# Kernel optimization log

Measured on AMD Instinct MI355X. Metric: run time of the kernel, lower is better.

Reference implementation:

```python
import jax, jax.numpy as jnp
import numpy as np

NUM_EMBEDDINGS = 1024
EMBEDDING_DIM = 64
COMMITMENT_COST = 0.25
EPS_NORM = 1e-12  # torch F.normalize eps


def _l2_normalize(x):
    n = jnp.linalg.norm(x, axis=-1, keepdims=True)
    return x / jnp.maximum(n, EPS_NORM)


def setup_inputs() -> dict:
    key = jax.random.key(0)
    k1, k2 = jax.random.split(key)
    inputs = jax.random.normal(k1, (16, 4096, EMBEDDING_DIM), dtype=jnp.float32)
    weight = jax.random.normal(k2, (NUM_EMBEDDINGS, EMBEDDING_DIM), dtype=jnp.float32) * 0.02
    return {"inputs": inputs, "weight": weight}


def reference(inputs, weight):
    input_shape = inputs.shape
    x = _l2_normalize(inputs)                      # [B,S,D]
    flat = x.reshape(-1, EMBEDDING_DIM)            # [N,D]
    w = _l2_normalize(weight)                      # [K,D]

    distances = (jnp.sum(flat ** 2, axis=1, keepdims=True)
                 + jnp.sum(w ** 2, axis=1)
                 - 2.0 * flat @ w.T)               # [N,K]
    encoding_indices = jnp.argmin(distances, axis=1)  # [N]

    quantized = w[encoding_indices].reshape(input_shape)  # [B,S,D]

    e_latent_loss = jnp.mean((jax.lax.stop_gradient(quantized) - x) ** 2)
    q_latent_loss = jnp.mean((quantized - jax.lax.stop_gradient(x)) ** 2)
    loss = q_latent_loss + COMMITMENT_COST * e_latent_loss

    # straight-through estimator
    quantized_ste = x + jax.lax.stop_gradient(quantized - x)

    # perplexity (no-grad bookkeeping)
    n = encoding_indices.shape[0]
    counts = jnp.zeros((NUM_EMBEDDINGS,), jnp.float32).at[encoding_indices].add(1.0)
    avg_probs = counts / n
    perplexity = jnp.exp(-jnp.sum(avg_probs * jnp.log(avg_probs + 1e-10)))

    return loss, quantized_ste, perplexity, encoding_indices[:, None]
```

## Files before the change

kernel.cpp:

```cpp
#include <hip/hip_runtime.h>
#include <hip/hip_bf16.h>
#include <math.h>

#define NROWS   65536
#define DIM     64
#define KCODES  1024
#define RPB     128
#define NBLOCKS (NROWS / RPB)

#define NEXACT 9u

typedef short short8 __attribute__((ext_vector_type(8)));
typedef float f32x4  __attribute__((ext_vector_type(4)));

#define OUT_Q_OFF    ((size_t)1)
#define OUT_PERP_OFF ((size_t)(1 + (size_t)NROWS * DIM))
#define OUT_IDX_OFF  ((size_t)(2 + (size_t)NROWS * DIM))

#define WS_COUNTS 0
#define WS_SSEC   4096
#define WS_DONE   4100
#define WS_WN     8192
#define WS_SK     (WS_WN + KCODES*DIM*4)
#define WS_WNH    (WS_SK + KCODES*4)
#define WS_WNL    (WS_WNH + KCODES*DIM*2)

__device__ __forceinline__ unsigned short bf16_rne(float f) {
  unsigned u = __float_as_uint(f);
  return (unsigned short)((u + 0x7FFFu + ((u >> 16) & 1u)) >> 16);
}
__device__ __forceinline__ float bf16f(unsigned short h) {
  return __uint_as_float(((unsigned)h) << 16);
}
__device__ __forceinline__ unsigned med3u(unsigned a, unsigned b, unsigned c) {
  unsigned d;
  asm("v_med3_u32 %0, %1, %2, %3" : "=v"(d) : "v"(a), "v"(b), "v"(c));
  return d;
}

__global__ void __launch_bounds__(64) normalize_w_kernel(
    const float* __restrict__ w, float* __restrict__ wn, float* __restrict__ sk,
    unsigned short* __restrict__ wnh, unsigned short* __restrict__ wnl,
    unsigned* __restrict__ counts, float* __restrict__ sse_accum,
    unsigned* __restrict__ done) {
  const int k = blockIdx.x;
  const int d = threadIdx.x;
  if (d == 0) {
    counts[k] = 0u;
    if (k == 0) { *sse_accum = 0.f; *done = 0u; }
  }
  float v = w[k * DIM + d];
  float ss = v * v;
  #pragma unroll
  for (int o = 32; o > 0; o >>= 1) ss += __shfl_xor(ss, o, 64);
  const float den = fmaxf(sqrtf(ss), 1e-12f);
  const float q = v / den;
  wn[k * DIM + d] = q;
  const unsigned short h = bf16_rne(q);
  wnh[k * DIM + d] = h;
  wnl[k * DIM + d] = bf16_rne(q - bf16f(h));
  float s2 = q * q;
  #pragma unroll
  for (int o = 32; o > 0; o >>= 1) s2 += __shfl_xor(s2, o, 64);
  if (d == 0) sk[k] = s2;
}

__global__ void __launch_bounds__(256) vq_mega_kernel(
    const float* __restrict__ x, const unsigned short* __restrict__ wnh,
    const unsigned short* __restrict__ wnl, const float* __restrict__ sk,
    const float* __restrict__ wn, float* __restrict__ out,
    unsigned* __restrict__ counts, float* __restrict__ sse_accum,
    unsigned* __restrict__ done) {
  __shared__ unsigned AB[9216];
  __shared__ float skb[2][64];
  __shared__ float c_arr[RPB];
  __shared__ float rowsse[RPB];
  __shared__ int   ib[RPB];
  __shared__ int   qlist[RPB];
  __shared__ int   flist[RPB];
  __shared__ int   qn_s, fn_s;
  __shared__ int   islast;
  const int tid = threadIdx.x;
  const int lane = tid & 63, wave = tid >> 6;

  if (tid == 0) { qn_s = 0; fn_s = 0; }

  {
    const int row_l = tid >> 1;
    const int half = tid & 1;
    const size_t row = (size_t)blockIdx.x * RPB + row_l;
    const float4* xr = (const float4*)(x + row * DIM) + half * 8;
    float4 xv[8];
    float ss = 0.f;
    #pragma unroll
    for (int i = 0; i < 8; i++) {
      xv[i] = xr[i];
      ss += xv[i].x * xv[i].x + xv[i].y * xv[i].y + xv[i].z * xv[i].z + xv[i].w * xv[i].w;
    }
    ss += __shfl_xor(ss, 1, 64);
    const float inv = 1.0f / fmaxf(sqrtf(ss), 1e-12f);
    float c = 0.f;
    #pragma unroll
    for (int i = 0; i < 8; i++) {
      const float a0 = xv[i].x * inv, a1 = xv[i].y * inv;
      const float a2 = xv[i].z * inv, a3 = xv[i].w * inv;
      c += a0 * a0 + a1 * a1 + a2 * a2 + a3 * a3;
      const unsigned short h0 = bf16_rne(a0), h1 = bf16_rne(a1);
      const unsigned short h2 = bf16_rne(a2), h3 = bf16_rne(a3);
      const unsigned short l0 = bf16_rne(a0 - bf16f(h0)), l1 = bf16_rne(a1 - bf16f(h1));
      const unsigned short l2 = bf16_rne(a2 - bf16f(h2)), l3 = bf16_rne(a3 - bf16f(h3));
      AB[row_l * 36 + half * 16 + 2 * i]            = (unsigned)h0 | ((unsigned)h1 << 16);
      AB[row_l * 36 + half * 16 + 2 * i + 1]        = (unsigned)h2 | ((unsigned)h3 << 16);
      AB[4608 + row_l * 36 + half * 16 + 2 * i]     = (unsigned)l0 | ((unsigned)l1 << 16);
      AB[4608 + row_l * 36 + half * 16 + 2 * i + 1] = (unsigned)l2 | ((unsigned)l3 << 16);
    }
    c += __shfl_xor(c, 1, 64);
    if (half == 0) c_arr[row_l] = c;
  }
  __syncthreads();

  short8 ah[2][2], al[2][2];
  #pragma unroll
  for (int rt = 0; rt < 2; rt++)
    #pragma unroll
    for (int kk = 0; kk < 2; kk++) {
      const int r = wave * 32 + rt * 16 + (lane & 15);
      ah[rt][kk] = *(const short8*)&AB[r * 36 + kk * 16 + (lane >> 4) * 4];
      al[rt][kk] = *(const short8*)&AB[4608 + r * 36 + kk * 16 + (lane >> 4) * 4];
    }
  __syncthreads();

  unsigned k1[8], k2[8], k3[8];
  #pragma unroll
  for (int s = 0; s < 8; s++) { k1[s] = 0xFFFFFFFFu; k2[s] = 0xFFFFFFFFu; k3[s] = 0xFFFFFFFFu; }

  {
    const int code = tid >> 2, q = tid & 3;
    const float4* gh = (const float4*)(wnh + (size_t)code * DIM + q * 16);
    const float4* gl = (const float4*)(wnl + (size_t)code * DIM + q * 16);
    float4* dh = (float4*)&AB[code * 36 + q * 8];
    float4* dl = (float4*)&AB[2304 + code * 36 + q * 8];
    dh[0] = gh[0]; dh[1] = gh[1];
    dl[0] = gl[0]; dl[1] = gl[1];
    if (tid < 64) skb[0][tid] = sk[tid] + 4.0f;
  }

  #pragma unroll 2
  for (int c = 0; c < 16; c++) {
    const int b = c & 1;
    __syncthreads();
    if (c < 15) {
      const int nb = b ^ 1;
      const int code = tid >> 2, q = tid & 3;
      const float4* gh = (const float4*)(wnh + (size_t)((c + 1) * 64 + code) * DIM + q * 16);
      const float4* gl = (const float4*)(wnl + (size_t)((c + 1) * 64 + code) * DIM + q * 16);
      float4* dh = (float4*)&AB[nb * 4608 + code * 36 + q * 8];
      float4* dl = (float4*)&AB[nb * 4608 + 2304 + code * 36 + q * 8];
      dh[0] = gh[0]; dh[1] = gh[1];
      dl[0] = gl[0]; dl[1] = gl[1];
      if (tid < 64) skb[nb][tid] = sk[(c + 1) * 64 + tid] + 4.0f;
    }
    #pragma unroll
    for (int tt = 0; tt < 4; tt++) {
      const int cb = tt * 16 + (lane & 15);
      const float skv4 = skb[b][cb];
      const unsigned chi = (unsigned)(c * 4 + tt);
      const short8 bh0 = *(const short8*)&AB[b * 4608 + cb * 36 + 0 * 16 + (lane >> 4) * 4];
      const short8 bh1 = *(const short8*)&AB[b * 4608 + cb * 36 + 1 * 16 + (lane >> 4) * 4];
      const short8 bl0 = *(const short8*)&AB[b * 4608 + 2304 + cb * 36 + 0 * 16 + (lane >> 4) * 4];
      const short8 bl1 = *(const short8*)&AB[b * 4608 + 2304 + cb * 36 + 1 * 16 + (lane >> 4) * 4];
      #pragma unroll
      for (int rt = 0; rt < 2; rt++) {
        f32x4 acc = {0.f, 0.f, 0.f, 0.f};
        acc = __builtin_amdgcn_mfma_f32_16x16x32_bf16(ah[rt][0], bh0, acc, 0, 0, 0);
        acc = __builtin_amdgcn_mfma_f32_16x16x32_bf16(ah[rt][1], bh1, acc, 0, 0, 0);
        acc = __builtin_amdgcn_mfma_f32_16x16x32_bf16(al[rt][0], bh0, acc, 0, 0, 0);
        acc = __builtin_amdgcn_mfma_f32_16x16x32_bf16(al[rt][1], bh1, acc, 0, 0, 0);
        acc = __builtin_amdgcn_mfma_f32_16x16x32_bf16(ah[rt][0], bl0, acc, 0, 0, 0);
        acc = __builtin_amdgcn_mfma_f32_16x16x32_bf16(ah[rt][1], bl1, acc, 0, 0, 0);
        #pragma unroll
        for (int i = 0; i < 4; i++) {
          const float dist4 = fmaf(-2.0f, acc[i], skv4);
          const unsigned key = (__float_as_uint(dist4) & 0xFFFFFFC0u) | chi;
          const int s = rt * 4 + i;
          const unsigned t = (k1[s] > key) ? k1[s] : key;
          k3[s] = med3u(k2[s], k3[s], t);
          k2[s] = med3u(k1[s], k2[s], key);
          k1[s] = (key < k1[s]) ? key : k1[s];
        }
      }
    }
  }

  #pragma unroll
  for (int s = 0; s < 8; s++) {
    unsigned a1 = (k1[s] << 4) | (unsigned)(lane & 15);
    unsigned a2 = (k2[s] << 4) | (unsigned)(lane & 15);
    unsigned a3 = (k3[s] << 4) | (unsigned)(lane & 15);
    #pragma unroll
    for (int m = 1; m < 16; m <<= 1) {
      const unsigned p1 = (unsigned)__shfl_xor((int)a1, m, 64);
      const unsigned p2 = (unsigned)__shfl_xor((int)a2, m, 64);
      const unsigned p3 = (unsigned)__shfl_xor((int)a3, m, 64);
      const unsigned th = (a1 > p1) ? a1 : p1;
      const unsigned n1 = (a1 < p1) ? a1 : p1;
      const unsigned m2 = (a2 < p2) ? a2 : p2;
      const unsigned m3 = (a3 < p3) ? a3 : p3;
      const unsigned hi = (th > m2) ? th : m2;
      a1 = n1;
      a2 = (th < m2) ? th : m2;
      const unsigned md = med3u(th, m2, m3);
      a3 = (hi < md) ? hi : md;
    }
    if ((lane & 15) == 0) {
      const int row_local = wave * 32 + (s >> 2) * 16 + (lane >> 4) * 4 + (s & 3);
      const int i1 = (int)(a1 & 1023u);
      ib[row_local] = i1;
      const unsigned ub = ((a1 & 0xFFFFFC00u) >> 4) | 0x40000000u;
      rowsse[row_local] = __uint_as_float(ub) - 4.0f + c_arr[row_local] + 1.6e-5f;
      const unsigned b1 = a1 >> 10, b2 = a2 >> 10, b3 = a3 >> 10;
      if (b3 - b1 < NEXACT) {
        flist[atomicAdd(&fn_s, 1)] = row_local;
      } else if (b2 - b1 < NEXACT) {
        qlist[atomicAdd(&qn_s, 1)] = row_local | (i1 << 7) | ((int)(a2 & 1023u) << 17);
      }
    }
  }
  __syncthreads();

  const int qn = qn_s, fn = fn_s;
  if (tid < qn) {
    const int packed = qlist[tid];
    const int rl = packed & 127;
    const int c1 = (packed >> 7) & 1023, c2i = (packed >> 17) & 1023;
    const size_t row = (size_t)blockIdx.x * RPB + rl;
    const float4* xr = (const float4*)(x + row * DIM);
    float4 xv[16];
    float ss = 0.f;
    #pragma unroll
    for (int i = 0; i < 16; i++) {
      xv[i] = xr[i];
      ss += xv[i].x * xv[i].x + xv[i].y * xv[i].y + xv[i].z * xv[i].z + xv[i].w * xv[i].w;
    }
    const float den = fmaxf(sqrtf(ss), 1e-12f);
    #pragma unroll
    for (int i = 0; i < 16; i++) { xv[i].x /= den; xv[i].y /= den; xv[i].z /= den; xv[i].w /= den; }
    float cc = 0.f;
    #pragma unroll
    for (int i = 0; i < 16; i++)
      cc += xv[i].x * xv[i].x + xv[i].y * xv[i].y + xv[i].z * xv[i].z + xv[i].w * xv[i].w;
    float dd[2]; const int cand[2] = {c1, c2i};
    #pragma unroll
    for (int t = 0; t < 2; t++) {
      const float4* wr = (const float4*)(wn + (size_t)cand[t] * DIM);
      float e0 = 0.f, e1 = 0.f, e2 = 0.f, e3 = 0.f;
      #pragma unroll
      for (int i = 0; i < 16; i++) {
        const float4 wv = wr[i];
        e0 = fmaf(xv[i].x, wv.x, e0);
        e1 = fmaf(xv[i].y, wv.y, e1);
        e2 = fmaf(xv[i].z, wv.z, e2);
        e3 = fmaf(xv[i].w, wv.w, e3);
      }
      dd[t] = (cc + sk[cand[t]]) - 2.0f * ((e0 + e1) + (e2 + e3));
    }
    const bool tb = (dd[1] < dd[0]) || (dd[1] == dd[0] && c2i < c1);
    ib[rl] = tb ? c2i : c1;
    rowsse[rl] = tb ? dd[1] : dd[0];
  }

  for (int qi = wave; qi < fn; qi += 4) {
    const int rl = flist[qi];
    const size_t row = (size_t)blockIdx.x * RPB + rl;
    const float4* xr = (const float4*)(x + row * DIM);
    float4 xv[16];
    float ss = 0.f;
    #pragma unroll
    for (int i = 0; i < 16; i++) {
      xv[i] = xr[i];
      ss += xv[i].x * xv[i].x + xv[i].y * xv[i].y + xv[i].z * xv[i].z + xv[i].w * xv[i].w;
    }
    const float den = fmaxf(sqrtf(ss), 1e-12f);
    #pragma unroll
    for (int i = 0; i < 16; i++) { xv[i].x /= den; xv[i].y /= den; xv[i].z /= den; xv[i].w /= den; }
    float cc = 0.f;
    #pragma unroll
    for (int i = 0; i < 16; i++)
      cc += xv[i].x * xv[i].x + xv[i].y * xv[i].y + xv[i].z * xv[i].z + xv[i].w * xv[i].w;

    float best = INFINITY;
    int bidx = 0x7FFFFFFF;
    for (int j = 0; j < 16; j++) {
      const int k = j * 64 + lane;
      const float4* wr = (const float4*)(wn + (size_t)k * DIM);
      float e0 = 0.f, e1 = 0.f, e2 = 0.f, e3 = 0.f;
      #pragma unroll
      for (int i = 0; i < 16; i++) {
        const float4 wv = wr[i];
        e0 = fmaf(xv[i].x, wv.x, e0);
        e1 = fmaf(xv[i].y, wv.y, e1);
        e2 = fmaf(xv[i].z, wv.z, e2);
        e3 = fmaf(xv[i].w, wv.w, e3);
      }
      const float dot = (e0 + e1) + (e2 + e3);
      const float dist = (cc + sk[k]) - 2.0f * dot;
      if (dist < best) { best = dist; bidx = k; }
    }
    #pragma unroll
    for (int m = 1; m < 64; m <<= 1) {
      const float pb = __shfl_xor(best, m, 64);
      const int pi = __shfl_xor(bidx, m, 64);
      if (pb < best || (pb == best && pi < bidx)) { best = pb; bidx = pi; }
    }
    if (lane == 0) { ib[rl] = bidx; rowsse[rl] = best; }
  }
  __syncthreads();

  if (tid < RPB) {
    const size_t row = (size_t)blockIdx.x * RPB + tid;
    const int idx = ib[tid];
    out[OUT_IDX_OFF + row] = (float)idx;
    atomicAdd(&counts[idx], 1u);
  }

  const size_t obase = OUT_Q_OFF + (size_t)blockIdx.x * (RPB * DIM);
  #pragma unroll 4
  for (int j = 0; j < 32; j++) {
    const int e = j * 256 + tid;
    out[obase + e] = wn[(size_t)ib[e >> 6] * DIM + (e & 63)];
  }

  __syncthreads();
  for (int s = 64; s > 0; s >>= 1) {
    if (tid < s) rowsse[tid] += rowsse[tid + s];
    __syncthreads();
  }
  if (tid == 0) atomicAdd(sse_accum, rowsse[0]);

  if (tid == 0) {
    __threadfence();
    islast = (atomicAdd(done, 1u) == NBLOCKS - 1) ? 1 : 0;
  }
  __syncthreads();
  if (islast) {
    __threadfence();
    float h = 0.f;
    #pragma unroll
    for (int i = 0; i < 4; i++) {
      const float cv = (float)counts[tid * 4 + i];
      const float avg = cv * (1.0f / (float)NROWS);
      h += avg * logf(avg + 1e-10f);
    }
    #pragma unroll
    for (int o = 32; o > 0; o >>= 1) h += __shfl_xor(h, o, 64);
    __shared__ float hred[4];
    if (lane == 0) hred[wave] = h;
    __syncthreads();
    if (tid == 0) {
      const float H = -(hred[0] + hred[1] + hred[2] + hred[3]);
      const float mse = *sse_accum * (1.0f / (float)((size_t)NROWS * DIM));
      out[0] = mse + 0.25f * mse;
      out[OUT_PERP_OFF] = expf(H);
    }
  }
}

extern "C" void kernel_launch(void* const* d_in, const int* in_sizes, int n_in,
                              void* d_out, int out_size, void* d_ws, size_t ws_size,
                              hipStream_t stream) {
  const float* x = (const float*)d_in[0];
  const float* w = (const float*)d_in[1];
  float* out = (float*)d_out;

  char* ws = (char*)d_ws;
  unsigned* counts    = (unsigned*)(ws + WS_COUNTS);
  float* sse_accum    = (float*)(ws + WS_SSEC);
  unsigned* done      = (unsigned*)(ws + WS_DONE);
  float* wn           = (float*)(ws + WS_WN);
  float* sk           = (float*)(ws + WS_SK);
  unsigned short* wnh = (unsigned short*)(ws + WS_WNH);
  unsigned short* wnl = (unsigned short*)(ws + WS_WNL);

  normalize_w_kernel<<<KCODES, 64, 0, stream>>>(w, wn, sk, wnh, wnl,
                                                counts, sse_accum, done);
  vq_mega_kernel<<<NBLOCKS, 256, 0, stream>>>(
      x, wnh, wnl, sk, wn, out, counts, sse_accum, done);
}
```

Before: 130.0 us.

## Double block to 512 threads, split codebook columns across wave pairs

Raises the block size from 256 to 512 threads. Each pair of waves now shares a row group, and each wave in the pair scans half of every 64-code chunk. The per-wave top-3 candidate keys are merged through shared memory in a new combine step before rows are classified for exact refinement. Loading and writeback loops are re-split across the extra threads. The goal is more waves per block to hide MFMA and LDS latency and to halve each wave's serial work, at the cost of an extra barrier, a merge pass, and possibly lower register budget under launch bounds of 4.

```diff
diff --git a/kernel.cpp b/kernel.cpp
--- a/kernel.cpp
+++ b/kernel.cpp
@@ -6,6 +6,7 @@
 #define DIM     64
 #define KCODES  1024
 #define RPB     128
+#define TPB     512
 #define NBLOCKS (NROWS / RPB)
 
 #define NEXACT 9u
@@ -37,6 +38,8 @@
   asm("v_med3_u32 %0, %1, %2, %3" : "=v"(d) : "v"(a), "v"(b), "v"(c));
   return d;
 }
+__device__ __forceinline__ unsigned uminu(unsigned a, unsigned b) { return a < b ? a : b; }
+__device__ __forceinline__ unsigned umaxu(unsigned a, unsigned b) { return a > b ? a : b; }
 
 __global__ void __launch_bounds__(64) normalize_w_kernel(
     const float* __restrict__ w, float* __restrict__ wn, float* __restrict__ sk,
@@ -65,13 +68,13 @@
   if (d == 0) sk[k] = s2;
 }
 
-__global__ void __launch_bounds__(256) vq_mega_kernel(
+__global__ void __launch_bounds__(TPB, 4) vq_mega_kernel(
     const float* __restrict__ x, const unsigned short* __restrict__ wnh,
     const unsigned short* __restrict__ wnl, const float* __restrict__ sk,
     const float* __restrict__ wn, float* __restrict__ out,
     unsigned* __restrict__ counts, float* __restrict__ sse_accum,
     unsigned* __restrict__ done) {
-  __shared__ unsigned AB[9216];
+  __shared__ __align__(16) unsigned AB[9216];
   __shared__ float skb[2][64];
   __shared__ float c_arr[RPB];
   __shared__ float rowsse[RPB];
@@ -80,28 +83,30 @@
   __shared__ int   flist[RPB];
   __shared__ int   qn_s, fn_s;
   __shared__ int   islast;
+  __shared__ float hred[8];
   const int tid = threadIdx.x;
   const int lane = tid & 63, wave = tid >> 6;
+  const int rg = wave >> 1, cg = wave & 1;
 
   if (tid == 0) { qn_s = 0; fn_s = 0; }
 
   {
-    const int row_l = tid >> 1;
-    const int half = tid & 1;
+    const int row_l = tid >> 2;
+    const int qr = tid & 3;
     const size_t row = (size_t)blockIdx.x * RPB + row_l;
-    const float4* xr = (const float4*)(x + row * DIM) + half * 8;
-    float4 xv[8];
+    const float4* xr = (const float4*)(x + row * DIM) + qr * 4;
+    float4 xv[4];
     float ss = 0.f;
     #pragma unroll
-    for (int i = 0; i < 8; i++) {
+    for (int i = 0; i < 4; i++) {
       xv[i] = xr[i];
       ss += xv[i].x * xv[i].x + xv[i].y * xv[i].y + xv[i].z * xv[i].z + xv[i].w * xv[i].w;
     }
-    ss += __shfl_xor(ss, 1, 64);
+    ss += __shfl_xor(ss, 1, 64); ss += __shfl_xor(ss, 2, 64);
     const float inv = 1.0f / fmaxf(sqrtf(ss), 1e-12f);
     float c = 0.f;
     #pragma unroll
-    for (int i = 0; i < 8; i++) {
+    for (int i = 0; i < 4; i++) {
       const float a0 = xv[i].x * inv, a1 = xv[i].y * inv;
       const float a2 = xv[i].z * inv, a3 = xv[i].w * inv;
       c += a0 * a0 + a1 * a1 + a2 * a2 + a3 * a3;
@@ -109,13 +114,13 @@
       const unsigned short h2 = bf16_rne(a2), h3 = bf16_rne(a3);
       const unsigned short l0 = bf16_rne(a0 - bf16f(h0)), l1 = bf16_rne(a1 - bf16f(h1));
       const unsigned short l2 = bf16_rne(a2 - bf16f(h2)), l3 = bf16_rne(a3 - bf16f(h3));
-      AB[row_l * 36 + half * 16 + 2 * i]            = (unsigned)h0 | ((unsigned)h1 << 16);
-      AB[row_l * 36 + half * 16 + 2 * i + 1]        = (unsigned)h2 | ((unsigned)h3 << 16);
-      AB[4608 + row_l * 36 + half * 16 + 2 * i]     = (unsigned)l0 | ((unsigned)l1 << 16);
-      AB[4608 + row_l * 36 + half * 16 + 2 * i + 1] = (unsigned)l2 | ((unsigned)l3 << 16);
-    }
-    c += __shfl_xor(c, 1, 64);
-    if (half == 0) c_arr[row_l] = c;
+      AB[row_l * 36 + qr * 8 + 2 * i]            = (unsigned)h0 | ((unsigned)h1 << 16);
+      AB[row_l * 36 + qr * 8 + 2 * i + 1]        = (unsigned)h2 | ((unsigned)h3 << 16);
+      AB[4608 + row_l * 36 + qr * 8 + 2 * i]     = (unsigned)l0 | ((unsigned)l1 << 16);
+      AB[4608 + row_l * 36 + qr * 8 + 2 * i + 1] = (unsigned)l2 | ((unsigned)l3 << 16);
+    }
+    c += __shfl_xor(c, 1, 64); c += __shfl_xor(c, 2, 64);
+    if (qr == 0) c_arr[row_l] = c;
   }
   __syncthreads();
 
@@ -124,7 +129,7 @@
   for (int rt = 0; rt < 2; rt++)
     #pragma unroll
     for (int kk = 0; kk < 2; kk++) {
-      const int r = wave * 32 + rt * 16 + (lane & 15);
+      const int r = rg * 32 + rt * 16 + (lane & 15);
       ah[rt][kk] = *(const short8*)&AB[r * 36 + kk * 16 + (lane >> 4) * 4];
       al[rt][kk] = *(const short8*)&AB[4608 + r * 36 + kk * 16 + (lane >> 4) * 4];
     }
@@ -135,13 +140,9 @@
   for (int s = 0; s < 8; s++) { k1[s] = 0xFFFFFFFFu; k2[s] = 0xFFFFFFFFu; k3[s] = 0xFFFFFFFFu; }
 
   {
-    const int code = tid >> 2, q = tid & 3;
-    const float4* gh = (const float4*)(wnh + (size_t)code * DIM + q * 16);
-    const float4* gl = (const float4*)(wnl + (size_t)code * DIM + q * 16);
-    float4* dh = (float4*)&AB[code * 36 + q * 8];
-    float4* dl = (float4*)&AB[2304 + code * 36 + q * 8];
-    dh[0] = gh[0]; dh[1] = gh[1];
-    dl[0] = gl[0]; dl[1] = gl[1];
+    const int code = tid >> 3, q = tid & 7;
+    *(float4*)&AB[code * 36 + q * 4]        = *(const float4*)(wnh + (size_t)code * DIM + q * 8);
+    *(float4*)&AB[2304 + code * 36 + q * 4] = *(const float4*)(wnl + (size_t)code * DIM + q * 8);
     if (tid < 64) skb[0][tid] = sk[tid] + 4.0f;
   }
 
@@ -151,20 +152,18 @@
     __syncthreads();
     if (c < 15) {
       const int nb = b ^ 1;
-      const int code = tid >> 2, q = tid & 3;
-      const float4* gh = (const float4*)(wnh + (size_t)((c + 1) * 64 + code) * DIM + q * 16);
-      const float4* gl = (const float4*)(wnl + (size_t)((c + 1) * 64 + code) * DIM + q * 16);
-      float4* dh = (float4*)&AB[nb * 4608 + code * 36 + q * 8];
-      float4* dl = (float4*)&AB[nb * 4608 + 2304 + code * 36 + q * 8];
-      dh[0] = gh[0]; dh[1] = gh[1];
-      dl[0] = gl[0]; dl[1] = gl[1];
+      const int code = tid >> 3, q = tid & 7;
+      *(float4*)&AB[nb * 4608 + code * 36 + q * 4] =
+          *(const float4*)(wnh + (size_t)((c + 1) * 64 + code) * DIM + q * 8);
+      *(float4*)&AB[nb * 4608 + 2304 + code * 36 + q * 4] =
+          *(const float4*)(wnl + (size_t)((c + 1) * 64 + code) * DIM + q * 8);
       if (tid < 64) skb[nb][tid] = sk[(c + 1) * 64 + tid] + 4.0f;
     }
     #pragma unroll
-    for (int tt = 0; tt < 4; tt++) {
-      const int cb = tt * 16 + (lane & 15);
+    for (int tt = 0; tt < 2; tt++) {
+      const int cb = cg * 32 + tt * 16 + (lane & 15);
       const float skv4 = skb[b][cb];
-      const unsigned chi = (unsigned)(c * 4 + tt);
+      const unsigned chi = (unsigned)(c * 4 + cg * 2 + tt);
       const short8 bh0 = *(const short8*)&AB[b * 4608 + cb * 36 + 0 * 16 + (lane >> 4) * 4];
       const short8 bh1 = *(const short8*)&AB[b * 4608 + cb * 36 + 1 * 16 + (lane >> 4) * 4];
       const short8 bl0 = *(const short8*)&AB[b * 4608 + 2304 + cb * 36 + 0 * 16 + (lane >> 4) * 4];
@@ -183,10 +182,10 @@
           const float dist4 = fmaf(-2.0f, acc[i], skv4);
           const unsigned key = (__float_as_uint(dist4) & 0xFFFFFFC0u) | chi;
           const int s = rt * 4 + i;
-          const unsigned t = (k1[s] > key) ? k1[s] : key;
+          const unsigned t = umaxu(k1[s], key);
           k3[s] = med3u(k2[s], k3[s], t);
           k2[s] = med3u(k1[s], k2[s], key);
-          k1[s] = (key < k1[s]) ? key : k1[s];
+          k1[s] = uminu(k1[s], key);
         }
       }
     }
@@ -202,28 +201,42 @@
       const unsigned p1 = (unsigned)__shfl_xor((int)a1, m, 64);
       const unsigned p2 = (unsigned)__shfl_xor((int)a2, m, 64);
       const unsigned p3 = (unsigned)__shfl_xor((int)a3, m, 64);
-      const unsigned th = (a1 > p1) ? a1 : p1;
-      const unsigned n1 = (a1 < p1) ? a1 : p1;
-      const unsigned m2 = (a2 < p2) ? a2 : p2;
-      const unsigned m3 = (a3 < p3) ? a3 : p3;
-      const unsigned hi = (th > m2) ? th : m2;
+      const unsigned th = umaxu(a1, p1);
+      const unsigned n1 = uminu(a1, p1);
+      const unsigned m2 = uminu(a2, p2);
+      const unsigned m3 = uminu(a3, p3);
+      const unsigned hi = umaxu(th, m2);
       a1 = n1;
-      a2 = (th < m2) ? th : m2;
-      const unsigned md = med3u(th, m2, m3);
-      a3 = (hi < md) ? hi : md;
+      a2 = uminu(th, m2);
+      a3 = uminu(hi, med3u(th, m2, m3));
     }
     if ((lane & 15) == 0) {
-      const int row_local = wave * 32 + (s >> 2) * 16 + (lane >> 4) * 4 + (s & 3);
-      const int i1 = (int)(a1 & 1023u);
-      ib[row_local] = i1;
-      const unsigned ub = ((a1 & 0xFFFFFC00u) >> 4) | 0x40000000u;
-      rowsse[row_local] = __uint_as_float(ub) - 4.0f + c_arr[row_local] + 1.6e-5f;
-      const unsigned b1 = a1 >> 10, b2 = a2 >> 10, b3 = a3 >> 10;
-      if (b3 - b1 < NEXACT) {
-        flist[atomicAdd(&fn_s, 1)] = row_local;
-      } else if (b2 - b1 < NEXACT) {
-        qlist[atomicAdd(&qn_s, 1)] = row_local | (i1 << 7) | ((int)(a2 & 1023u) << 17);
-      }
+      const int row_local = rg * 32 + (s >> 2) * 16 + (lane >> 4) * 4 + (s & 3);
+      AB[cg * 384 + row_local * 3 + 0] = a1;
+      AB[cg * 384 + row_local * 3 + 1] = a2;
+      AB[cg * 384 + row_local * 3 + 2] = a3;
+    }
+  }
+  __syncthreads();
+
+  if (tid < RPB) {
+    const unsigned x1 = AB[tid * 3 + 0], x2 = AB[tid * 3 + 1], x3 = AB[tid * 3 + 2];
+    const unsigned y1 = AB[384 + tid * 3 + 0], y2 = AB[384 + tid * 3 + 1],
+                   y3 = AB[384 + tid * 3 + 2];
+    const unsigned m1 = uminu(x1, y1);
+    const unsigned t1 = umaxu(x1, y1);
+    const unsigned u  = uminu(x2, y2);
+    const unsigned m2 = uminu(t1, u);
+    const unsigned m3 = med3u(t1, u, uminu(umaxu(x2, y2), uminu(x3, y3)));
+    const int i1 = (int)(m1 & 1023u);
+    ib[tid] = i1;
+    const unsigned ub = ((m1 & 0xFFFFFC00u) >> 4) | 0x40000000u;
+    rowsse[tid] = __uint_as_float(ub) - 4.0f + c_arr[tid] + 1.6e-5f;
+    const unsigned b1 = m1 >> 10, b2 = m2 >> 10, b3 = m3 >> 10;
+    if (b3 - b1 < NEXACT) {
+      flist[atomicAdd(&fn_s, 1)] = tid;
+    } else if (b2 - b1 < NEXACT) {
+      qlist[atomicAdd(&qn_s, 1)] = tid | (i1 << 7) | ((int)(m2 & 1023u) << 17);
     }
   }
   __syncthreads();
@@ -269,7 +282,7 @@
     rowsse[rl] = tb ? dd[1] : dd[0];
   }
 
-  for (int qi = wave; qi < fn; qi += 4) {
+  for (int qi = wave; qi < fn; qi += 8) {
     const int rl = flist[qi];
     const size_t row = (size_t)blockIdx.x * RPB + rl;
     const float4* xr = (const float4*)(x + row * DIM);
@@ -325,8 +338,8 @@
 
   const size_t obase = OUT_Q_OFF + (size_t)blockIdx.x * (RPB * DIM);
   #pragma unroll 4
-  for (int j = 0; j < 32; j++) {
-    const int e = j * 256 + tid;
+  for (int j = 0; j < 16; j++) {
+    const int e = j * TPB + tid;
     out[obase + e] = wn[(size_t)ib[e >> 6] * DIM + (e & 63)];
   }
 
@@ -346,18 +359,18 @@
     __threadfence();
     float h = 0.f;
     #pragma unroll
-    for (int i = 0; i < 4; i++) {
-      const float cv = (float)counts[tid * 4 + i];
+    for (int i = 0; i < 2; i++) {
+      const float cv = (float)counts[tid * 2 + i];
       const float avg = cv * (1.0f / (float)NROWS);
       h += avg * logf(avg + 1e-10f);
     }
     #pragma unroll
     for (int o = 32; o > 0; o >>= 1) h += __shfl_xor(h, o, 64);
-    __shared__ float hred[4];
     if (lane == 0) hred[wave] = h;
     __syncthreads();
     if (tid == 0) {
-      const float H = -(hred[0] + hred[1] + hred[2] + hred[3]);
+      const float H = -(hred[0] + hred[1] + hred[2] + hred[3] +
+                        hred[4] + hred[5] + hred[6] + hred[7]);
       const float mse = *sse_accum * (1.0f / (float)((size_t)NROWS * DIM));
       out[0] = mse + 0.25f * mse;
       out[OUT_PERP_OFF] = expf(H);
@@ -383,6 +396,6 @@
 
   normalize_w_kernel<<<KCODES, 64, 0, stream>>>(w, wn, sk, wnh, wnl,
                                                 counts, sse_accum, done);
-  vq_mega_kernel<<<NBLOCKS, 256, 0, stream>>>(
+  vq_mega_kernel<<<NBLOCKS, TPB, 0, stream>>>(
       x, wnh, wnl, sk, wn, out, counts, sse_accum, done);
 }
```

New measurement: 132.4 us. No clear change (+1.9%).
